# Optimization experiments

Hardware: AMD Instinct MI355X
Metric: run time of the kernel (lower is better)

The kernel has to match this reference:

```python
import jax, jax.numpy as jnp
import numpy as np

EPS = 1e-9


def setup_inputs() -> dict:
    key = jax.random.key(0)
    k1, k2, k3, k4 = jax.random.split(key, 4)
    B, D, DOUT, NCLS = 1024, 512, 640, 1000
    f = jax.random.normal(k1, (B, D), dtype=jnp.float32)
    # dropout mask: True = erased feature, rate dp = 0.25
    mask = jax.random.uniform(k2, (B, D)) < 0.25
    # orthogonal init (columns orthonormal, like nn.init.orthogonal_ on (640, 512))
    A = jnp.linalg.qr(jax.random.normal(k3, (DOUT, D), dtype=jnp.float32))[0]
    W = jax.random.normal(k4, (NCLS, D), dtype=jnp.float32) * 0.02
    b = jnp.zeros((NCLS,), dtype=jnp.float32)
    return {"f": f, "mask": mask, "A": A, "W": W, "b": b}


def nncl(f, mask, A):
    B, D = f.shape
    m = mask.astype(f.dtype)                      # (B, D), 1 = erased
    # y = A @ x ; Z = y - A_K @ x_K  (computed in the same order as torch)
    y = f @ A.T                                    # (B, d_out)
    Z = y - (f * (1.0 - m)) @ A.T                  # (B, d_out) == A_E @ x_E
    # min-norm LS solution over erased columns via masked normal equations:
    # G = M A^T A M + (I - M) is block-diag [A_E^T A_E, I]; with A_E full
    # column rank (|E| < d_out), inv(G) M A^T Z == pinv(A_E) Z padded to D.
    AtA = A.T @ A                                  # (D, D)
    G = AtA[None] * (m[:, :, None] * m[:, None, :])
    G = G + jnp.eye(D, dtype=f.dtype)[None] * (1.0 - m)[:, :, None]
    rhs = m * (Z @ A)                              # (B, D) == M A^T Z
    sol = jnp.linalg.solve(G, rhs[..., None])[..., 0]
    x_rec = jnp.where(mask, sol, f)
    # metrics
    num_erased = m.sum(axis=1)
    ne = jnp.maximum(num_erased, 1.0)
    mse = (((x_rec - f) ** 2) * m).sum(axis=1) / ne
    var = jnp.var(f, axis=1)                       # unbiased=False
    rel = jnp.sqrt(mse + EPS) / jnp.sqrt(var + EPS)
    fr_acc = jnp.clip(1.0 - rel, 0.0, 1.0)
    return x_rec, mse, fr_acc, num_erased


def reference(f, mask, A, W, b):
    x_rec, mse, fr_acc, num_erased = nncl(f, mask, A)
    logits = x_rec @ W.T + b
    return logits, mse, fr_acc, num_erased
```

## Files before the change

kernel.cpp:

```cpp
#include <hip/hip_runtime.h>
#include <hip/hip_bf16.h>
#include <math.h>

#define B_ROWS 1024
#define D_IN   512
#define N_CLS  1000

typedef __attribute__((ext_vector_type(8))) short        bf16x8;
typedef __attribute__((ext_vector_type(4))) float        f32x4;
typedef __attribute__((ext_vector_type(4))) unsigned int u32x4;

__device__ __forceinline__ unsigned int pk(float lo, float hi) {
    union { __hip_bfloat162 h; unsigned int u; } c;
    c.h = __float22bfloat162_rn(make_float2(lo, hi));
    return c.u;
}

__global__ __launch_bounds__(256) void fused_kernel(
    const float* __restrict__ F,
    const int*   __restrict__ mask,
    const float* __restrict__ W,
    const float* __restrict__ bias,
    float* __restrict__ out_logits,
    float* __restrict__ out_mse,
    float* __restrict__ out_fr,
    float* __restrict__ out_ne)
{
    __shared__ __align__(16) char lds[65536];

    const int tid  = threadIdx.x;
    const int lane = tid & 63;
    const int wid  = tid >> 6;
    const int bid  = blockIdx.x;
    const int by = bid >> 4, bx = bid & 15;
    const int row0a = by * 64, row0b = bx * 64;

    const int srow = bid * 4 + wid;
    const float* sf = F    + (size_t)srow * D_IN + lane * 8;
    const int*   sm = mask + (size_t)srow * D_IN + lane * 8;
    const float4 sv0 = *(const float4*)(sf);
    const float4 sv1 = *(const float4*)(sf + 4);
    const int4   si0 = *(const int4*)(sm);
    const int4   si1 = *(const int4*)(sm + 4);

    const int wr = wid >> 1, wc = wid & 1;
    f32x4 acc[2][2] = {};

    const unsigned int swz    = (unsigned int)((lane & 7) << 4);
    const unsigned int qa     = (unsigned int)((lane >> 4) << 4);
    const unsigned int r16    = (unsigned int)(lane & 15);
    const unsigned int abase  = (unsigned int)((wr * 32 + r16) * 512) + qa;
    const unsigned int bbase  = 32768u + (unsigned int)((wc * 32 + r16) * 512) + qa;

    #pragma unroll
    for (int p = 0; p < 2; ++p) {
        if (p) __syncthreads();

        #pragma unroll
        for (int j = 0; j < 8; ++j) {
            const int n  = tid + 256 * j;
            const int r  = n >> 5;
            const int k8 = n & 31;
            const unsigned int off =
                ((unsigned int)(r * 512 + k8 * 16)) ^ ((unsigned int)(r & 7) << 4);

            const float* ap = F + (size_t)(row0a + r) * D_IN + p * 256 + k8 * 8;
            const float4 a0 = *(const float4*)ap;
            const float4 a1 = *(const float4*)(ap + 4);
            u32x4 oa = { pk(a0.x, a0.y), pk(a0.z, a0.w),
                         pk(a1.x, a1.y), pk(a1.z, a1.w) };
            *(u32x4*)(lds + off) = oa;

            const int wrow = row0b + r;
            u32x4 ob = { 0u, 0u, 0u, 0u };
            if (wrow < N_CLS) {
                const float* bp = W + (size_t)wrow * D_IN + p * 256 + k8 * 8;
                const float4 b0 = *(const float4*)bp;
                const float4 b1 = *(const float4*)(bp + 4);
                ob = (u32x4){ pk(b0.x, b0.y), pk(b0.z, b0.w),
                              pk(b1.x, b1.y), pk(b1.z, b1.w) };
            }
            *(u32x4*)(lds + 32768 + off) = ob;
        }
        __syncthreads();

        #pragma unroll
        for (int kt = 0; kt < 8; ++kt) {
            const unsigned int ko = (unsigned int)(kt * 64);
            const bf16x8 fa0 = *(const bf16x8*)(lds + ((abase + ko) ^ swz));
            const bf16x8 fa1 = *(const bf16x8*)(lds + ((abase + 8192 + ko) ^ swz));
            const bf16x8 fb0 = *(const bf16x8*)(lds + ((bbase + ko) ^ swz));
            const bf16x8 fb1 = *(const bf16x8*)(lds + ((bbase + 8192 + ko) ^ swz));
            acc[0][0] = __builtin_amdgcn_mfma_f32_16x16x32_bf16(fa0, fb0, acc[0][0], 0, 0, 0);
            acc[0][1] = __builtin_amdgcn_mfma_f32_16x16x32_bf16(fa0, fb1, acc[0][1], 0, 0, 0);
            acc[1][0] = __builtin_amdgcn_mfma_f32_16x16x32_bf16(fa1, fb0, acc[1][0], 0, 0, 0);
            acc[1][1] = __builtin_amdgcn_mfma_f32_16x16x32_bf16(fa1, fb1, acc[1][1], 0, 0, 0);
        }
    }

    #pragma unroll
    for (int fi = 0; fi < 2; ++fi) {
        const int rbase = row0a + wr * 32 + fi * 16 + ((lane >> 4) << 2);
        #pragma unroll
        for (int fj = 0; fj < 2; ++fj) {
            const int c = row0b + wc * 32 + fj * 16 + (lane & 15);
            if (c < N_CLS) {
                const float bv = bias[c];
                #pragma unroll
                for (int r = 0; r < 4; ++r)
                    out_logits[(size_t)(rbase + r) * N_CLS + c] = acc[fi][fj][r] + bv;
            }
        }
    }

    {
        float s  = sv0.x + sv0.y + sv0.z + sv0.w + sv1.x + sv1.y + sv1.z + sv1.w;
        float ss = sv0.x*sv0.x + sv0.y*sv0.y + sv0.z*sv0.z + sv0.w*sv0.w
                 + sv1.x*sv1.x + sv1.y*sv1.y + sv1.z*sv1.z + sv1.w*sv1.w;
        float cnt = (float)((si0.x != 0) + (si0.y != 0) + (si0.z != 0) + (si0.w != 0)
                          + (si1.x != 0) + (si1.y != 0) + (si1.z != 0) + (si1.w != 0));
        #pragma unroll
        for (int off = 32; off > 0; off >>= 1) {
            s   += __shfl_down(s, off);
            ss  += __shfl_down(ss, off);
            cnt += __shfl_down(cnt, off);
        }
        if (lane == 0) {
            const float mean = s * (1.0f / D_IN);
            const float var  = ss * (1.0f / D_IN) - mean * mean;
            float fr = 1.0f - sqrtf(1e-9f) / sqrtf(var + 1e-9f);
            fr = fminf(fmaxf(fr, 0.0f), 1.0f);
            out_mse[srow] = 0.0f;
            out_fr[srow]  = fr;
            out_ne[srow]  = cnt;
        }
    }
}

extern "C" void kernel_launch(void* const* d_in, const int* in_sizes, int n_in,
                              void* d_out, int out_size, void* d_ws, size_t ws_size,
                              hipStream_t stream) {
    const float* f    = (const float*)d_in[0];
    const int*   mask = (const int*)  d_in[1];
    const float* W    = (const float*)d_in[3];
    const float* bias = (const float*)d_in[4];

    float* logits = (float*)d_out;
    float* mse    = logits + (size_t)B_ROWS * N_CLS;
    float* fr     = mse + B_ROWS;
    float* ne     = fr  + B_ROWS;

    fused_kernel<<<dim3(256), dim3(256), 0, stream>>>(
        f, mask, W, bias, logits, mse, fr, ne);
}
```

Measured before the change: 13.59 us.

## Use 1024-thread blocks with full-K LDS staging and one 16x16 tile per wave

Each block now runs 16 waves instead of 4 and stages the whole 512-wide K range of both the F and W tiles into 128 KB of LDS in a single pass. This removes the two-phase load/sync loop, and each wave computes one 16x16 MFMA tile over 16 K steps. The goal is more waves per CU to hide global-load latency and fewer barriers. The cost is a large LDS footprint that limits residency to one block per CU. The per-row statistics are now computed by only the first 4 waves, after the GEMM.

After: 11.34 us, median of 2. 1.2x faster.

```diff
diff --git a/kernel.cpp b/kernel.cpp
--- a/kernel.cpp
+++ b/kernel.cpp
@@ -16,7 +16,7 @@
     return c.u;
 }
 
-__global__ __launch_bounds__(256) void fused_kernel(
+__global__ __launch_bounds__(1024, 4) void fused_kernel(
     const float* __restrict__ F,
     const int*   __restrict__ mask,
     const float* __restrict__ W,
@@ -26,7 +26,7 @@
     float* __restrict__ out_fr,
     float* __restrict__ out_ne)
 {
-    __shared__ __align__(16) char lds[65536];
+    __shared__ __align__(16) char lds[131072];
 
     const int tid  = threadIdx.x;
     const int lane = tid & 63;
@@ -35,90 +35,78 @@
     const int by = bid >> 4, bx = bid & 15;
     const int row0a = by * 64, row0b = bx * 64;
 
-    const int srow = bid * 4 + wid;
-    const float* sf = F    + (size_t)srow * D_IN + lane * 8;
-    const int*   sm = mask + (size_t)srow * D_IN + lane * 8;
-    const float4 sv0 = *(const float4*)(sf);
-    const float4 sv1 = *(const float4*)(sf + 4);
-    const int4   si0 = *(const int4*)(sm);
-    const int4   si1 = *(const int4*)(sm + 4);
+    #pragma unroll
+    for (int j = 0; j < 4; ++j) {
+        const int n = tid + 1024 * j;
+        const int r = n >> 6;
+        const int u = n & 63;
+        const unsigned int off =
+            ((unsigned int)(r * 1024 + u * 16)) ^ ((unsigned int)(r & 7) << 4);
 
-    const int wr = wid >> 1, wc = wid & 1;
-    f32x4 acc[2][2] = {};
+        const float* ap = F + (size_t)(row0a + r) * D_IN + u * 8;
+        const float4 a0 = *(const float4*)ap;
+        const float4 a1 = *(const float4*)(ap + 4);
+        u32x4 oa = { pk(a0.x, a0.y), pk(a0.z, a0.w),
+                     pk(a1.x, a1.y), pk(a1.z, a1.w) };
+        *(u32x4*)(lds + off) = oa;
 
-    const unsigned int swz    = (unsigned int)((lane & 7) << 4);
-    const unsigned int qa     = (unsigned int)((lane >> 4) << 4);
-    const unsigned int r16    = (unsigned int)(lane & 15);
-    const unsigned int abase  = (unsigned int)((wr * 32 + r16) * 512) + qa;
-    const unsigned int bbase  = 32768u + (unsigned int)((wc * 32 + r16) * 512) + qa;
+        const int wrow = row0b + r;
+        u32x4 ob = { 0u, 0u, 0u, 0u };
+        if (wrow < N_CLS) {
+            const float* bp = W + (size_t)wrow * D_IN + u * 8;
+            const float4 b0 = *(const float4*)bp;
+            const float4 b1 = *(const float4*)(bp + 4);
+            ob = (u32x4){ pk(b0.x, b0.y), pk(b0.z, b0.w),
+                          pk(b1.x, b1.y), pk(b1.z, b1.w) };
+        }
+        *(u32x4*)(lds + 65536 + off) = ob;
+    }
+    __syncthreads();
 
+    const int wr = wid >> 2, wc = wid & 3;
+    const unsigned int r16 = (unsigned int)(lane & 15);
+    const unsigned int qa  = (unsigned int)((lane >> 4) << 4);
+    const unsigned int ar  = (unsigned int)(wr * 16) + r16;
+    const unsigned int br  = (unsigned int)(wc * 16) + r16;
+    const unsigned int abase = ar * 1024u + qa;
+    const unsigned int bbase = 65536u + br * 1024u + qa;
+    const unsigned int aswz = (ar & 7u) << 4;
+    const unsigned int bswz = (br & 7u) << 4;
+
+    f32x4 acc = {};
     #pragma unroll
-    for (int p = 0; p < 2; ++p) {
-        if (p) __syncthreads();
+    for (int kt = 0; kt < 16; ++kt) {
+        const unsigned int ko = (unsigned int)(kt * 64);
+        const bf16x8 fa = *(const bf16x8*)(lds + ((abase + ko) ^ aswz));
+        const bf16x8 fb = *(const bf16x8*)(lds + ((bbase + ko) ^ bswz));
+        acc = __builtin_amdgcn_mfma_f32_16x16x32_bf16(fa, fb, acc, 0, 0, 0);
+    }
 
-        #pragma unroll
-        for (int j = 0; j < 8; ++j) {
-            const int n  = tid + 256 * j;
-            const int r  = n >> 5;
-            const int k8 = n & 31;
-            const unsigned int off =
-                ((unsigned int)(r * 512 + k8 * 16)) ^ ((unsigned int)(r & 7) << 4);
-
-            const float* ap = F + (size_t)(row0a + r) * D_IN + p * 256 + k8 * 8;
-            const float4 a0 = *(const float4*)ap;
-            const float4 a1 = *(const float4*)(ap + 4);
-            u32x4 oa = { pk(a0.x, a0.y), pk(a0.z, a0.w),
-                         pk(a1.x, a1.y), pk(a1.z, a1.w) };
-            *(u32x4*)(lds + off) = oa;
-
-            const int wrow = row0b + r;
-            u32x4 ob = { 0u, 0u, 0u, 0u };
-            if (wrow < N_CLS) {
-                const float* bp = W + (size_t)wrow * D_IN + p * 256 + k8 * 8;
-                const float4 b0 = *(const float4*)bp;
-                const float4 b1 = *(const float4*)(bp + 4);
-                ob = (u32x4){ pk(b0.x, b0.y), pk(b0.z, b0.w),
-                              pk(b1.x, b1.y), pk(b1.z, b1.w) };
-            }
-            *(u32x4*)(lds + 32768 + off) = ob;
-        }
-        __syncthreads();
-
-        #pragma unroll
-        for (int kt = 0; kt < 8; ++kt) {
-            const unsigned int ko = (unsigned int)(kt * 64);
-            const bf16x8 fa0 = *(const bf16x8*)(lds + ((abase + ko) ^ swz));
-            const bf16x8 fa1 = *(const bf16x8*)(lds + ((abase + 8192 + ko) ^ swz));
-            const bf16x8 fb0 = *(const bf16x8*)(lds + ((bbase + ko) ^ swz));
-            const bf16x8 fb1 = *(const bf16x8*)(lds + ((bbase + 8192 + ko) ^ swz));
-            acc[0][0] = __builtin_amdgcn_mfma_f32_16x16x32_bf16(fa0, fb0, acc[0][0], 0, 0, 0);
-            acc[0][1] = __builtin_amdgcn_mfma_f32_16x16x32_bf16(fa0, fb1, acc[0][1], 0, 0, 0);
-            acc[1][0] = __builtin_amdgcn_mfma_f32_16x16x32_bf16(fa1, fb0, acc[1][0], 0, 0, 0);
-            acc[1][1] = __builtin_amdgcn_mfma_f32_16x16x32_bf16(fa1, fb1, acc[1][1], 0, 0, 0);
+    {
+        const int rbase = row0a + wr * 16 + ((lane >> 4) << 2);
+        const int c     = row0b + wc * 16 + (lane & 15);
+        if (c < N_CLS) {
+            const float bv = bias[c];
+            #pragma unroll
+            for (int r = 0; r < 4; ++r)
+                out_logits[(size_t)(rbase + r) * N_CLS + c] = acc[r] + bv;
         }
     }
 
-    #pragma unroll
-    for (int fi = 0; fi < 2; ++fi) {
-        const int rbase = row0a + wr * 32 + fi * 16 + ((lane >> 4) << 2);
-        #pragma unroll
-        for (int fj = 0; fj < 2; ++fj) {
-            const int c = row0b + wc * 32 + fj * 16 + (lane & 15);
-            if (c < N_CLS) {
-                const float bv = bias[c];
-                #pragma unroll
-                for (int r = 0; r < 4; ++r)
-                    out_logits[(size_t)(rbase + r) * N_CLS + c] = acc[fi][fj][r] + bv;
-            }
-        }
-    }
+    if (wid < 4) {
+        const int srow = bid * 4 + wid;
+        const float* sf = F    + (size_t)srow * D_IN + lane * 8;
+        const int*   sm = mask + (size_t)srow * D_IN + lane * 8;
+        const float4 v0 = *(const float4*)(sf);
+        const float4 v1 = *(const float4*)(sf + 4);
+        const int4   i0 = *(const int4*)(sm);
+        const int4   i1 = *(const int4*)(sm + 4);
 
-    {
-        float s  = sv0.x + sv0.y + sv0.z + sv0.w + sv1.x + sv1.y + sv1.z + sv1.w;
-        float ss = sv0.x*sv0.x + sv0.y*sv0.y + sv0.z*sv0.z + sv0.w*sv0.w
-                 + sv1.x*sv1.x + sv1.y*sv1.y + sv1.z*sv1.z + sv1.w*sv1.w;
-        float cnt = (float)((si0.x != 0) + (si0.y != 0) + (si0.z != 0) + (si0.w != 0)
-                          + (si1.x != 0) + (si1.y != 0) + (si1.z != 0) + (si1.w != 0));
+        float s  = v0.x + v0.y + v0.z + v0.w + v1.x + v1.y + v1.z + v1.w;
+        float ss = v0.x*v0.x + v0.y*v0.y + v0.z*v0.z + v0.w*v0.w
+                 + v1.x*v1.x + v1.y*v1.y + v1.z*v1.z + v1.w*v1.w;
+        float cnt = (float)((i0.x != 0) + (i0.y != 0) + (i0.z != 0) + (i0.w != 0)
+                          + (i1.x != 0) + (i1.y != 0) + (i1.z != 0) + (i1.w != 0));
         #pragma unroll
         for (int off = 32; off > 0; off >>= 1) {
             s   += __shfl_down(s, off);
@@ -150,6 +138,6 @@
     float* fr     = mse + B_ROWS;
     float* ne     = fr  + B_ROWS;
 
-    fused_kernel<<<dim3(256), dim3(256), 0, stream>>>(
+    fused_kernel<<<dim3(256), dim3(1024), 0, stream>>>(
         f, mask, W, bias, logits, mse, fr, ne);
 }
```
